# Kernel tuning notes

Measured on AMD Instinct MI355X. Metric: run time of the kernel, lower is better.

The kernel has to match this reference:

```python
import jax, jax.numpy as jnp
import numpy as np

K = 2          # superpatch hop size (init kwarg)
BN_EPS = 1e-5  # torch BatchNorm2d default eps


def setup_inputs() -> dict:
    key = jax.random.key(0)
    ks = jax.random.split(key, 7)
    B, C, H, W = 32, 192, 56, 56
    Co = 2 * C  # out_channels must equal 2*in_channels for the BN to type-check
    x = jax.random.normal(ks[0], (B, C, H, W), jnp.float32)
    # 1x1 conv: weight [Co, 2C] (kernel dims squeezed), bias [Co]
    W_conv = jax.random.normal(ks[1], (Co, 2 * C), jnp.float32) * (1.0 / np.sqrt(2 * C))
    b_conv = jax.random.normal(ks[2], (Co,), jnp.float32) * 0.02
    # BatchNorm2d(2C) affine params + running stats (inference mode)
    gamma = 1.0 + 0.1 * jax.random.normal(ks[3], (Co,), jnp.float32)
    beta = 0.1 * jax.random.normal(ks[4], (Co,), jnp.float32)
    run_mean = 0.1 * jax.random.normal(ks[5], (Co,), jnp.float32)
    run_var = jax.random.uniform(ks[6], (Co,), jnp.float32, 0.5, 1.5)
    return {"x": x, "W_conv": W_conv, "b_conv": b_conv, "gamma": gamma,
            "beta": beta, "run_mean": run_mean, "run_var": run_var}


def _max_relative(x0, axis, n_steps):
    """Accumulate max(0, x0 - roll(x0, -i*K, axis)) for i=1..n_steps via scan.
    Carry keeps the running rolled tensor so each step rolls by only -K."""
    def step(carry, _):
        xr, xj = carry
        xr = jnp.roll(xr, -K, axis=axis)
        xj = jnp.maximum(xj, x0 - xr)
        return (xr, xj), None
    (_, xj), _ = jax.lax.scan(step, (x0, jnp.zeros_like(x0)), None, length=n_steps)
    return xj


def reference(x, W_conv, b_conv, gamma, beta, run_mean, run_var):
    B, C, H, W = x.shape
    # center the superpatch: roll by -(K//2) in both spatial dims
    x0 = jnp.roll(x, (-(K // 2), -(K // 2)), axis=(2, 3))
    # max-relative aggregation over row shifts then column shifts
    # torch.arange(K, H, K) has (H-1)//K elements
    xj_h = _max_relative(x0, axis=2, n_steps=(H - 1) // K)
    xj_w = _max_relative(x0, axis=3, n_steps=(W - 1) // K)
    xj = jnp.maximum(xj_h, xj_w)  # both loops fold into the same running max (init 0)
    xc = jnp.concatenate([x0, xj], axis=1)              # [B, 2C, H, W]
    xc = jnp.roll(xc, (K // 2, K // 2), axis=(2, 3))    # undo the centering roll
    # 1x1 conv == per-pixel GEMM
    y = jnp.einsum('bchw,oc->bohw', xc, W_conv) + b_conv[None, :, None, None]
    # BatchNorm2d in inference mode (running stats)
    scale = gamma * jax.lax.rsqrt(run_var + BN_EPS)
    y = y * scale[None, :, None, None] + (beta - run_mean * scale)[None, :, None, None]
    return jax.nn.gelu(y, approximate=False)  # torch nn.GELU default = exact erf
```

## Files before the change

### kernel.cpp

```cpp
#include <hip/hip_runtime.h>
#include <cstdint>

#define B_N 32
#define C_N 192
#define W_N 56
#define HW_N 3136
#define CO_N 384
#define K_N 384
#define M_N 100352

typedef unsigned short u16;
typedef unsigned int u32;
typedef __attribute__((ext_vector_type(8))) short short8;
typedef __attribute__((ext_vector_type(4))) float floatx4;

__device__ __forceinline__ u16 bf16rne(float f) {
  union { float f; u32 u; } v; v.f = f;
  u32 r = (v.u + 0x7FFFu + ((v.u >> 16) & 1u)) >> 16;
  return (u16)r;
}

__device__ __forceinline__ void stage16(const void* g, void* lbase, int lane) {
#if __has_builtin(__builtin_amdgcn_global_load_lds)
  __builtin_amdgcn_global_load_lds(
      (const __attribute__((address_space(1))) void*)(uintptr_t)g,
      (__attribute__((address_space(3))) void*)(u32)(uintptr_t)lbase,
      16, 0, 0);
#else
  *(uint4*)((char*)lbase + lane * 16) = *(const uint4*)g;
#endif
}

__global__ __launch_bounds__(256) void prep_consts(
    const float* __restrict__ Wc, const float* __restrict__ bconv,
    const float* __restrict__ gamma, const float* __restrict__ beta,
    const float* __restrict__ rmean, const float* __restrict__ rvar,
    u16* __restrict__ Wbf, float* __restrict__ alphaV, float* __restrict__ betaV) {
  int idx = blockIdx.x * 256 + threadIdx.x;
  if (idx < CO_N * K_N) Wbf[idx] = bf16rne(Wc[idx]);
  if (idx < CO_N) {
    float s = gamma[idx] * rsqrtf(rvar[idx] + 1e-5f);
    alphaV[idx] = s;
    betaV[idx] = bconv[idx] * s + beta[idx] - rmean[idx] * s;
  }
}

__global__ __launch_bounds__(256) void xj_compute(const float* __restrict__ x,
                                                  u16* __restrict__ XJ) {
  __shared__ float pl[HW_N];
  __shared__ float rmin1[112], rmin2[112], cmin1[112], cmin2[112];
  __shared__ int rarg[112], carg[112];
  int tid = threadIdx.x;
  size_t base = (size_t)blockIdx.x * HW_N;
  const float4* xp4 = (const float4*)(x + base);
  #pragma unroll 1
  for (int i = tid; i < HW_N / 4; i += 256) ((float4*)pl)[i] = xp4[i];
  __syncthreads();
  if (tid < 112) {
    int ww = tid >> 1, p = tid & 1;
    float m1 = 3e38f, m2 = 3e38f; int am = -1;
    #pragma unroll
    for (int j = 0; j < 28; ++j) {
      int h = p + 2 * j;
      float v = pl[h * W_N + ww];
      if (v < m1) { m2 = m1; m1 = v; am = h; } else if (v < m2) m2 = v;
    }
    rmin1[tid] = m1; rmin2[tid] = m2; rarg[tid] = am;
  } else if (tid < 224) {
    int t = tid - 112;
    int hh = t >> 1, p = t & 1;
    float m1 = 3e38f, m2 = 3e38f; int am = -1;
    #pragma unroll
    for (int j = 0; j < 28; ++j) {
      int wv = p + 2 * j;
      float v = pl[hh * W_N + wv];
      if (v < m1) { m2 = m1; m1 = v; am = wv; } else if (v < m2) m2 = v;
    }
    cmin1[t] = m1; cmin2[t] = m2; carg[t] = am;
  }
  __syncthreads();
  u16* op = XJ + base;
  #pragma unroll 1
  for (int i4 = tid; i4 < HW_N / 4; i4 += 256) {
    int idx = i4 * 4;
    int h = idx / W_N;
    int w0 = idx - h * W_N;
    ushort4 r;
    u16* rp = &r.x;
    #pragma unroll
    for (int j = 0; j < 4; ++j) {
      int wv = w0 + j;
      float v = pl[idx + j];
      int rt = (wv << 1) | (h & 1);
      float rm = (rarg[rt] == h) ? rmin2[rt] : rmin1[rt];
      int ct = (h << 1) | (wv & 1);
      float cm = (carg[ct] == wv) ? cmin2[ct] : cmin1[ct];
      float xj = v - fminf(rm, cm);
      rp[j] = bf16rne(fmaxf(xj, 0.0f));
    }
    *(ushort4*)(op + idx) = r;
  }
}


__global__ __launch_bounds__(512) void gemm_fused(
    const float* __restrict__ x, const u16* __restrict__ XJ,
    const u16* __restrict__ Wbf,
    const float* __restrict__ alphaV, const float* __restrict__ betaV,
    float* __restrict__ out) {
  __shared__ __align__(16) char smem_raw[65536];
  u16* As = (u16*)smem_raw;
  u32* As32 = (u32*)smem_raw;
  u16* Bs = (u16*)(smem_raw + 16384);
  float* ep = (float*)smem_raw;
  int tid = threadIdx.x;
  int lane = tid & 63;
  int w = tid >> 6;
  int wm = w & 1, wn = w >> 1;
  int l15 = lane & 15, quad = lane >> 4;
  int m0 = blockIdx.x << 7;

  int kp = tid >> 4;
  int pxq = tid & 15;
  u32 offs[2];
  #pragma unroll
  for (int r = 0; r < 2; ++r) {
    int gm = m0 + (pxq + 16 * r) * 4;
    int bb = gm / HW_N;
    int pp = gm - bb * HW_N;
    offs[r] = (u32)bb * (u32)(C_N * HW_N) + (u32)pp;
  }
  int lrow = lane >> 3;
  int lchunk = lane & 7;

  floatx4 acc[4][6];
  #pragma unroll
  for (int i = 0; i < 4; ++i)
    #pragma unroll
    for (int j = 0; j < 6; ++j) acc[i][j] = (floatx4)0.0f;

  #pragma unroll 1
  for (int ko = 0; ko < 3; ++ko) {
    int c0 = ko * 64;
    u32 pk[2][4];
    #pragma unroll
    for (int r = 0; r < 2; ++r) {
      const float* a = x + (size_t)offs[r] + (size_t)(c0 + 2 * kp) * HW_N;
      float4 v0 = *(const float4*)a;
      float4 v1 = *(const float4*)(a + HW_N);
      const float* f0 = &v0.x; const float* f1 = &v1.x;
      #pragma unroll
      for (int j = 0; j < 4; ++j)
        pk[r][j] = (u32)bf16rne(f0[j]) | ((u32)bf16rne(f1[j]) << 16);
    }
    __syncthreads();
    #pragma unroll
    for (int c = 0; c < 6; ++c) {
      int rowbase = w * 48 + c * 8;
      int row = rowbase + lrow;
      int chunk = lchunk ^ (row & 7);
      stage16(Wbf + (size_t)row * K_N + c0 + chunk * 8, Bs + rowbase * 64, lane);
    }
    #pragma unroll
    for (int r = 0; r < 2; ++r) {
      #pragma unroll
      for (int j = 0; j < 4; ++j) {
        int px = (pxq + 16 * r) * 4 + j;
        As32[px * 32 + (kp & 3) + (((kp >> 2) ^ ((px >> 1) & 7)) << 2)] = pk[r][j];
      }
    }
    __syncthreads();
    #pragma unroll
    for (int h2 = 0; h2 < 2; ++h2) {
      short8 aF[4], bF[6];
      #pragma unroll
      for (int mi = 0; mi < 4; ++mi) {
        int r = wm * 64 + mi * 16 + l15;
        aF[mi] = *(const short8*)(As + r * 64 + (((h2 * 4 + quad) ^ ((r >> 1) & 7)) << 3));
      }
      #pragma unroll
      for (int ni = 0; ni < 6; ++ni) {
        int r = wn * 96 + ni * 16 + l15;
        bF[ni] = *(const short8*)(Bs + r * 64 + (((h2 * 4 + quad) ^ (r & 7)) << 3));
      }
      #pragma unroll
      for (int mi = 0; mi < 4; ++mi)
        #pragma unroll
        for (int ni = 0; ni < 6; ++ni)
          acc[mi][ni] = __builtin_amdgcn_mfma_f32_16x16x32_bf16(
              aF[mi], bF[ni], acc[mi][ni], 0, 0, 0);
    }
  }

  #pragma unroll 1
  for (int ko = 0; ko < 3; ++ko) {
    int c0 = ko * 64;
    u32 pk[2][4];
    #pragma unroll
    for (int r = 0; r < 2; ++r) {
      const u16* a = XJ + (size_t)offs[r] + (size_t)(c0 + 2 * kp) * HW_N;
      ushort4 v0 = *(const ushort4*)a;
      ushort4 v1 = *(const ushort4*)(a + HW_N);
      const u16* q0 = &v0.x; const u16* q1 = &v1.x;
      #pragma unroll
      for (int j = 0; j < 4; ++j)
        pk[r][j] = (u32)q0[j] | ((u32)q1[j] << 16);
    }
    __syncthreads();
    #pragma unroll
    for (int c = 0; c < 6; ++c) {
      int rowbase = w * 48 + c * 8;
      int row = rowbase + lrow;
      int chunk = lchunk ^ (row & 7);
      stage16(Wbf + (size_t)row * K_N + 192 + c0 + chunk * 8, Bs + rowbase * 64, lane);
    }
    #pragma unroll
    for (int r = 0; r < 2; ++r) {
      #pragma unroll
      for (int j = 0; j < 4; ++j) {
        int px = (pxq + 16 * r) * 4 + j;
        As32[px * 32 + (kp & 3) + (((kp >> 2) ^ ((px >> 1) & 7)) << 2)] = pk[r][j];
      }
    }
    __syncthreads();
    #pragma unroll
    for (int h2 = 0; h2 < 2; ++h2) {
      short8 aF[4], bF[6];
      #pragma unroll
      for (int mi = 0; mi < 4; ++mi) {
        int r = wm * 64 + mi * 16 + l15;
        aF[mi] = *(const short8*)(As + r * 64 + (((h2 * 4 + quad) ^ ((r >> 1) & 7)) << 3));
      }
      #pragma unroll
      for (int ni = 0; ni < 6; ++ni) {
        int r = wn * 96 + ni * 16 + l15;
        bF[ni] = *(const short8*)(Bs + r * 64 + (((h2 * 4 + quad) ^ (r & 7)) << 3));
      }
      #pragma unroll
      for (int mi = 0; mi < 4; ++mi)
        #pragma unroll
        for (int ni = 0; ni < 6; ++ni)
          acc[mi][ni] = __builtin_amdgcn_mfma_f32_16x16x32_bf16(
              aF[mi], bF[ni], acc[mi][ni], 0, 0, 0);
    }
  }

  float av[6], bv[6];
  #pragma unroll
  for (int ni = 0; ni < 6; ++ni) {
    int o = wn * 96 + ni * 16 + l15;
    av[ni] = alphaV[o];
    bv[ni] = betaV[o];
  }
  #pragma unroll 1
  for (int oc = 0; oc < 4; ++oc) {
    __syncthreads();
    if (wn == oc) {
      #pragma unroll
      for (int ni = 0; ni < 6; ++ni) {
        #pragma unroll
        for (int mi = 0; mi < 4; ++mi) {
          floatx4 a = acc[mi][ni];
          float4 g;
          float* gp = &g.x;
          #pragma unroll
          for (int i = 0; i < 4; ++i) {
            float t = a[i] * av[ni] + bv[ni];
            gp[i] = 0.5f * t * (1.0f + erff(t * 0.70710678118654752f));
          }
          *(float4*)&ep[(ni * 16 + l15) * 132 + wm * 64 + mi * 16 + quad * 4] = g;
        }
      }
    }
    __syncthreads();
    #pragma unroll
    for (int it = 0; it < 6; ++it) {
      int task = tid + it * 512;
      int r = task >> 5;
      int c4 = task & 31;
      float4 v = *(float4*)&ep[r * 132 + c4 * 4];
      int gm = m0 + c4 * 4;
      int bb = gm / HW_N;
      int pp = gm - bb * HW_N;
      *(float4*)(out + ((size_t)(bb * CO_N + oc * 96 + r)) * HW_N + pp) = v;
    }
  }
}

extern "C" void kernel_launch(void* const* d_in, const int* in_sizes, int n_in,
                              void* d_out, int out_size, void* d_ws, size_t ws_size,
                              hipStream_t stream) {
  const float* x  = (const float*)d_in[0];
  const float* Wc = (const float*)d_in[1];
  const float* bc = (const float*)d_in[2];
  const float* gm = (const float*)d_in[3];
  const float* bt = (const float*)d_in[4];
  const float* rm = (const float*)d_in[5];
  const float* rv = (const float*)d_in[6];
  float* out = (float*)d_out;

  char* ws = (char*)d_ws;
  size_t offXJ = 0;
  size_t offWb = offXJ + (size_t)B_N * C_N * HW_N * 2;
  size_t offAl = offWb + (size_t)CO_N * K_N * 2;
  u16* XJ = (u16*)(ws + offXJ);
  u16* Wbf = (u16*)(ws + offWb);
  float* alphaV = (float*)(ws + offAl);
  float* betaV = alphaV + CO_N;

  hipLaunchKernelGGL(prep_consts, dim3(576), dim3(256), 0, stream,
                     Wc, bc, gm, bt, rm, rv, Wbf, alphaV, betaV);
  hipLaunchKernelGGL(xj_compute, dim3(B_N * C_N), dim3(256), 0, stream, x, XJ);
  hipLaunchKernelGGL(gemm_fused, dim3(M_N / 128), dim3(512), 0, stream,
                     x, XJ, Wbf, alphaV, betaV, out);
}
```

Before: 350.6 us.

## Rework xj kernel per-wave and prefetch A tiles, read weights from global

The xj kernel now processes one plane per wave, two waves per block, using a padded LDS layout and wave-level barriers instead of block syncs. Each lane computes both row and column two-smallest minima. The GEMM merges its two K loops into one six-step loop that prefetches the next A tile into registers during the MFMAs. It drops LDS staging of the weights and reads B fragments straight from global/L2, with a smaller LDS footprint and a launch bound aiming for more resident blocks. This trades LDS traffic for uncoalesced global weight reads, which may hurt if L2 hit latency dominates.

```diff
diff --git a/kernel.cpp b/kernel.cpp
--- a/kernel.cpp
+++ b/kernel.cpp
@@ -18,17 +18,6 @@
   union { float f; u32 u; } v; v.f = f;
   u32 r = (v.u + 0x7FFFu + ((v.u >> 16) & 1u)) >> 16;
   return (u16)r;
-}
-
-__device__ __forceinline__ void stage16(const void* g, void* lbase, int lane) {
-#if __has_builtin(__builtin_amdgcn_global_load_lds)
-  __builtin_amdgcn_global_load_lds(
-      (const __attribute__((address_space(1))) void*)(uintptr_t)g,
-      (__attribute__((address_space(3))) void*)(u32)(uintptr_t)lbase,
-      16, 0, 0);
-#else
-  *(uint4*)((char*)lbase + lane * 16) = *(const uint4*)g;
-#endif
 }
 
 __global__ __launch_bounds__(256) void prep_consts(
@@ -45,73 +34,136 @@
   }
 }
 
-__global__ __launch_bounds__(256) void xj_compute(const float* __restrict__ x,
+#define PLN_F 3192
+#define WSLOT 3864
+
+__global__ __launch_bounds__(128) void xj_compute(const float* __restrict__ x,
                                                   u16* __restrict__ XJ) {
-  __shared__ float pl[HW_N];
-  __shared__ float rmin1[112], rmin2[112], cmin1[112], cmin2[112];
-  __shared__ int rarg[112], carg[112];
+  __shared__ float sm[2 * WSLOT];
   int tid = threadIdx.x;
-  size_t base = (size_t)blockIdx.x * HW_N;
-  const float4* xp4 = (const float4*)(x + base);
+  int wid = tid >> 6, lane = tid & 63;
+  float* pl  = sm + wid * WSLOT;
+  float* rs1 = pl + PLN_F;
+  float* rs2 = rs1 + 112;
+  float* rsa = rs2 + 112;
+  float* cs1 = rsa + 112;
+  float* cs2 = cs1 + 112;
+  float* csa = cs2 + 112;
+  size_t base = ((size_t)blockIdx.x * 2 + wid) * HW_N;
+  const float4* xg4 = (const float4*)(x + base);
+
   #pragma unroll 1
-  for (int i = tid; i < HW_N / 4; i += 256) ((float4*)pl)[i] = xp4[i];
-  __syncthreads();
-  if (tid < 112) {
-    int ww = tid >> 1, p = tid & 1;
-    float m1 = 3e38f, m2 = 3e38f; int am = -1;
-    #pragma unroll
-    for (int j = 0; j < 28; ++j) {
-      int h = p + 2 * j;
-      float v = pl[h * W_N + ww];
-      if (v < m1) { m2 = m1; m1 = v; am = h; } else if (v < m2) m2 = v;
-    }
-    rmin1[tid] = m1; rmin2[tid] = m2; rarg[tid] = am;
-  } else if (tid < 224) {
-    int t = tid - 112;
-    int hh = t >> 1, p = t & 1;
-    float m1 = 3e38f, m2 = 3e38f; int am = -1;
-    #pragma unroll
-    for (int j = 0; j < 28; ++j) {
-      int wv = p + 2 * j;
-      float v = pl[hh * W_N + wv];
-      if (v < m1) { m2 = m1; m1 = v; am = wv; } else if (v < m2) m2 = v;
-    }
-    cmin1[t] = m1; cmin2[t] = m2; carg[t] = am;
-  }
-  __syncthreads();
+  for (int i = lane; i < 784; i += 64) {
+    float4 v = xg4[i];
+    int h = i / 14;
+    int w0 = (i - h * 14) * 4;
+    float* d = pl + h * 57 + w0;
+    d[0] = v.x; d[1] = v.y; d[2] = v.z; d[3] = v.w;
+  }
+  asm volatile("s_waitcnt lgkmcnt(0)" ::: "memory");
+  __builtin_amdgcn_wave_barrier();
+
+  if (lane < 56) {
+    float m1a = 3e38f, m2a = 3e38f, m1b = 3e38f, m2b = 3e38f;
+    int aa = -1, ab = -1;
+    #pragma unroll
+    for (int h = 0; h < 56; h += 2) {
+      float va = pl[h * 57 + lane];
+      float vb = pl[(h + 1) * 57 + lane];
+      if (va < m1a) { m2a = m1a; m1a = va; aa = h; } else m2a = fminf(m2a, va);
+      if (vb < m1b) { m2b = m1b; m1b = vb; ab = h + 1; } else m2b = fminf(m2b, vb);
+    }
+    rs1[lane] = m1a; rs1[56 + lane] = m1b;
+    rs2[lane] = m2a; rs2[56 + lane] = m2b;
+    rsa[lane] = __int_as_float(aa); rsa[56 + lane] = __int_as_float(ab);
+
+    m1a = 3e38f; m2a = 3e38f; m1b = 3e38f; m2b = 3e38f; aa = -1; ab = -1;
+    const float* rowp = pl + lane * 57;
+    #pragma unroll
+    for (int w = 0; w < 56; w += 2) {
+      float va = rowp[w];
+      float vb = rowp[w + 1];
+      if (va < m1a) { m2a = m1a; m1a = va; aa = w; } else m2a = fminf(m2a, va);
+      if (vb < m1b) { m2b = m1b; m1b = vb; ab = w + 1; } else m2b = fminf(m2b, vb);
+    }
+    cs1[lane] = m1a; cs1[56 + lane] = m1b;
+    cs2[lane] = m2a; cs2[56 + lane] = m2b;
+    csa[lane] = __int_as_float(aa); csa[56 + lane] = __int_as_float(ab);
+  }
+  asm volatile("s_waitcnt lgkmcnt(0)" ::: "memory");
+  __builtin_amdgcn_wave_barrier();
+
   u16* op = XJ + base;
   #pragma unroll 1
-  for (int i4 = tid; i4 < HW_N / 4; i4 += 256) {
-    int idx = i4 * 4;
-    int h = idx / W_N;
-    int w0 = idx - h * W_N;
-    ushort4 r;
-    u16* rp = &r.x;
+  for (int i = lane; i < 784; i += 64) {
+    int idx = i * 4;
+    int h = i / 14;
+    int w0 = (i - h * 14) * 4;
+    int hp = h & 1;
+    const float* pr = pl + h * 57 + w0;
+    float4 r1 = *(const float4*)(rs1 + hp * 56 + w0);
+    float4 r2 = *(const float4*)(rs2 + hp * 56 + w0);
+    float4 ra = *(const float4*)(rsa + hp * 56 + w0);
+    float c1a = cs1[h], c1b = cs1[56 + h];
+    float c2a = cs2[h], c2b = cs2[56 + h];
+    int caa = __float_as_int(csa[h]), cab = __float_as_int(csa[56 + h]);
+    ushort4 o;
+    u16* opx = &o.x;
+    const float* r1p = &r1.x; const float* r2p = &r2.x; const float* rap = &ra.x;
     #pragma unroll
     for (int j = 0; j < 4; ++j) {
       int wv = w0 + j;
-      float v = pl[idx + j];
-      int rt = (wv << 1) | (h & 1);
-      float rm = (rarg[rt] == h) ? rmin2[rt] : rmin1[rt];
-      int ct = (h << 1) | (wv & 1);
-      float cm = (carg[ct] == wv) ? cmin2[ct] : cmin1[ct];
-      float xj = v - fminf(rm, cm);
-      rp[j] = bf16rne(fmaxf(xj, 0.0f));
-    }
-    *(ushort4*)(op + idx) = r;
-  }
-}
-
-
-__global__ __launch_bounds__(512) void gemm_fused(
+      float rm = (__float_as_int(rap[j]) == h) ? r2p[j] : r1p[j];
+      float cm;
+      if ((wv & 1) == 0) cm = (caa == wv) ? c2a : c1a;
+      else               cm = (cab == wv) ? c2b : c1b;
+      float xj = pr[j] - fminf(rm, cm);
+      opx[j] = bf16rne(fmaxf(xj, 0.0f));
+    }
+    *(ushort4*)(op + idx) = o;
+  }
+}
+
+
+__device__ __forceinline__ void load_pk(int s, u32 pk[2][4],
+                                        const float* __restrict__ x,
+                                        const u16* __restrict__ XJ,
+                                        const u32* offs, int kp) {
+  if (s < 3) {
+    int c0 = s * 64;
+    #pragma unroll
+    for (int r = 0; r < 2; ++r) {
+      const float* a = x + (size_t)offs[r] + (size_t)(c0 + 2 * kp) * HW_N;
+      float4 v0 = *(const float4*)a;
+      float4 v1 = *(const float4*)(a + HW_N);
+      const float* f0 = &v0.x; const float* f1 = &v1.x;
+      #pragma unroll
+      for (int j = 0; j < 4; ++j)
+        pk[r][j] = (u32)bf16rne(f0[j]) | ((u32)bf16rne(f1[j]) << 16);
+    }
+  } else {
+    int c0 = (s - 3) * 64;
+    #pragma unroll
+    for (int r = 0; r < 2; ++r) {
+      const u16* a = XJ + (size_t)offs[r] + (size_t)(c0 + 2 * kp) * HW_N;
+      ushort4 v0 = *(const ushort4*)a;
+      ushort4 v1 = *(const ushort4*)(a + HW_N);
+      const u16* q0 = &v0.x; const u16* q1 = &v1.x;
+      #pragma unroll
+      for (int j = 0; j < 4; ++j)
+        pk[r][j] = (u32)q0[j] | ((u32)q1[j] << 16);
+    }
+  }
+}
+
+__global__ __launch_bounds__(512, 4) void gemm_fused(
     const float* __restrict__ x, const u16* __restrict__ XJ,
     const u16* __restrict__ Wbf,
     const float* __restrict__ alphaV, const float* __restrict__ betaV,
     float* __restrict__ out) {
-  __shared__ __align__(16) char smem_raw[65536];
+  __shared__ __align__(16) char smem_raw[50688];
   u16* As = (u16*)smem_raw;
   u32* As32 = (u32*)smem_raw;
-  u16* Bs = (u16*)(smem_raw + 16384);
   float* ep = (float*)smem_raw;
   int tid = threadIdx.x;
   int lane = tid & 63;
@@ -130,8 +182,6 @@
     int pp = gm - bb * HW_N;
     offs[r] = (u32)bb * (u32)(C_N * HW_N) + (u32)pp;
   }
-  int lrow = lane >> 3;
-  int lchunk = lane & 7;
 
   floatx4 acc[4][6];
   #pragma unroll
@@ -139,28 +189,12 @@
     #pragma unroll
     for (int j = 0; j < 6; ++j) acc[i][j] = (floatx4)0.0f;
 
+  u32 pk[2][4];
+  load_pk(0, pk, x, XJ, offs, kp);
+
   #pragma unroll 1
-  for (int ko = 0; ko < 3; ++ko) {
-    int c0 = ko * 64;
-    u32 pk[2][4];
-    #pragma unroll
-    for (int r = 0; r < 2; ++r) {
-      const float* a = x + (size_t)offs[r] + (size_t)(c0 + 2 * kp) * HW_N;
-      float4 v0 = *(const float4*)a;
-      float4 v1 = *(const float4*)(a + HW_N);
-      const float* f0 = &v0.x; const float* f1 = &v1.x;
-      #pragma unroll
-      for (int j = 0; j < 4; ++j)
-        pk[r][j] = (u32)bf16rne(f0[j]) | ((u32)bf16rne(f1[j]) << 16);
-    }
+  for (int ko = 0; ko < 6; ++ko) {
     __syncthreads();
-    #pragma unroll
-    for (int c = 0; c < 6; ++c) {
-      int rowbase = w * 48 + c * 8;
-      int row = rowbase + lrow;
-      int chunk = lchunk ^ (row & 7);
-      stage16(Wbf + (size_t)row * K_N + c0 + chunk * 8, Bs + rowbase * 64, lane);
-    }
     #pragma unroll
     for (int r = 0; r < 2; ++r) {
       #pragma unroll
@@ -170,6 +204,9 @@
       }
     }
     __syncthreads();
+    u32 pkn[2][4];
+    if (ko < 5) load_pk(ko + 1, pkn, x, XJ, offs, kp);
+    int k0 = ko * 64;
     #pragma unroll
     for (int h2 = 0; h2 < 2; ++h2) {
       short8 aF[4], bF[6];
@@ -181,7 +218,7 @@
       #pragma unroll
       for (int ni = 0; ni < 6; ++ni) {
         int r = wn * 96 + ni * 16 + l15;
-        bF[ni] = *(const short8*)(Bs + r * 64 + (((h2 * 4 + quad) ^ (r & 7)) << 3));
+        bF[ni] = *(const short8*)(Wbf + (size_t)r * K_N + k0 + ((h2 * 4 + quad) << 3));
       }
       #pragma unroll
       for (int mi = 0; mi < 4; ++mi)
@@ -190,58 +227,11 @@
           acc[mi][ni] = __builtin_amdgcn_mfma_f32_16x16x32_bf16(
               aF[mi], bF[ni], acc[mi][ni], 0, 0, 0);
     }
-  }
-
-  #pragma unroll 1
-  for (int ko = 0; ko < 3; ++ko) {
-    int c0 = ko * 64;
-    u32 pk[2][4];
-    #pragma unroll
-    for (int r = 0; r < 2; ++r) {
-      const u16* a = XJ + (size_t)offs[r] + (size_t)(c0 + 2 * kp) * HW_N;
-      ushort4 v0 = *(const ushort4*)a;
-      ushort4 v1 = *(const ushort4*)(a + HW_N);
-      const u16* q0 = &v0.x; const u16* q1 = &v1.x;
-      #pragma unroll
-      for (int j = 0; j < 4; ++j)
-        pk[r][j] = (u32)q0[j] | ((u32)q1[j] << 16);
-    }
-    __syncthreads();
-    #pragma unroll
-    for (int c = 0; c < 6; ++c) {
-      int rowbase = w * 48 + c * 8;
-      int row = rowbase + lrow;
-      int chunk = lchunk ^ (row & 7);
-      stage16(Wbf + (size_t)row * K_N + 192 + c0 + chunk * 8, Bs + rowbase * 64, lane);
-    }
-    #pragma unroll
-    for (int r = 0; r < 2; ++r) {
-      #pragma unroll
-      for (int j = 0; j < 4; ++j) {
-        int px = (pxq + 16 * r) * 4 + j;
-        As32[px * 32 + (kp & 3) + (((kp >> 2) ^ ((px >> 1) & 7)) << 2)] = pk[r][j];
-      }
-    }
-    __syncthreads();
-    #pragma unroll
-    for (int h2 = 0; h2 < 2; ++h2) {
-      short8 aF[4], bF[6];
-      #pragma unroll
-      for (int mi = 0; mi < 4; ++mi) {
-        int r = wm * 64 + mi * 16 + l15;
-        aF[mi] = *(const short8*)(As + r * 64 + (((h2 * 4 + quad) ^ ((r >> 1) & 7)) << 3));
-      }
-      #pragma unroll
-      for (int ni = 0; ni < 6; ++ni) {
-        int r = wn * 96 + ni * 16 + l15;
-        bF[ni] = *(const short8*)(Bs + r * 64 + (((h2 * 4 + quad) ^ (r & 7)) << 3));
-      }
-      #pragma unroll
-      for (int mi = 0; mi < 4; ++mi)
+    if (ko < 5) {
+      #pragma unroll
+      for (int r = 0; r < 2; ++r)
         #pragma unroll
-        for (int ni = 0; ni < 6; ++ni)
-          acc[mi][ni] = __builtin_amdgcn_mfma_f32_16x16x32_bf16(
-              aF[mi], bF[ni], acc[mi][ni], 0, 0, 0);
+        for (int j = 0; j < 4; ++j) pk[r][j] = pkn[r][j];
     }
   }
 
@@ -310,7 +300,7 @@
 
   hipLaunchKernelGGL(prep_consts, dim3(576), dim3(256), 0, stream,
                      Wc, bc, gm, bt, rm, rv, Wbf, alphaV, betaV);
-  hipLaunchKernelGGL(xj_compute, dim3(B_N * C_N), dim3(256), 0, stream, x, XJ);
+  hipLaunchKernelGGL(xj_compute, dim3(B_N * C_N / 2), dim3(128), 0, stream, x, XJ);
   hipLaunchKernelGGL(gemm_fused, dim3(M_N / 128), dim3(512), 0, stream,
                      x, XJ, Wbf, alphaV, betaV, out);
 }
```

Result: slower. 499.1 us (+42.4%).
